# Kernel optimization log

Hardware: AMD Instinct MI355X
Metric: run time of the kernel (lower is better)

Reference implementation:

```python
import jax, jax.numpy as jnp
import numpy as np

B, S, D, H = 2, 2048, 1024, 16
HD = D // H  # head_dim = 64
INIT_STD = 0.02


def rotate_half(x):
    half = x.shape[-1] // 2
    return jnp.concatenate((-x[..., half:], x[..., :half]), axis=-1)


def setup_inputs() -> dict:
    key = jax.random.key(0)
    ks = jax.random.split(key, 6)
    inputs_q = jax.random.normal(ks[0], (B, S, D), dtype=jnp.float32)
    # causal mask, shape [B, 1, S, S] (broadcasts over heads)
    mask = jnp.broadcast_to(jnp.tril(jnp.ones((S, S), dtype=bool))[None, None], (B, 1, S, S))
    Wq = jax.random.normal(ks[1], (D, D), dtype=jnp.float32) * INIT_STD
    Wk = jax.random.normal(ks[2], (D, D), dtype=jnp.float32) * INIT_STD
    Wv = jax.random.normal(ks[3], (D, D), dtype=jnp.float32) * INIT_STD
    Wo = jax.random.normal(ks[4], (D, D), dtype=jnp.float32) * INIT_STD
    bq = jnp.zeros((D,), jnp.float32)
    bk = jnp.zeros((D,), jnp.float32)
    bv = jnp.zeros((D,), jnp.float32)
    bo = jnp.zeros((D,), jnp.float32)
    return {"inputs_q": inputs_q, "mask": mask, "Wq": Wq, "bq": bq, "Wk": Wk, "bk": bk,
            "Wv": Wv, "bv": bv, "Wo": Wo, "bo": bo}


def reference(inputs_q, mask, Wq, bq, Wk, bk, Wv, bv, Wo, bo):
    b, s, d = inputs_q.shape
    h, hd = H, d // H
    # QKV projections, split heads -> [b, s, h, hd]
    q = (inputs_q @ Wq + bq).reshape(b, s, h, hd)
    k = (inputs_q @ Wk + bk).reshape(b, s, h, hd)
    v = (inputs_q @ Wv + bv).reshape(b, s, h, hd)
    # rotary position embedding (GPT-J/Llama style: duplicated freqs over halves)
    pos = jnp.arange(s, dtype=jnp.float32)
    inv_freq = 1.0 / (10000.0 ** (jnp.arange(0, hd, 2, dtype=jnp.float32) / hd))
    freqs = pos[:, None] * inv_freq[None, :]              # [s, hd//2]
    emb = jnp.concatenate((freqs, freqs), axis=-1)        # [s, hd]
    sin = jnp.sin(emb)[None, :, None, :]                  # [1, s, 1, hd]
    cos = jnp.cos(emb)[None, :, None, :]
    q = q * cos + rotate_half(q) * sin
    k = k * cos + rotate_half(k) * sin
    # additive attention bias from boolean mask
    bias = jnp.where(mask, 0.0, jnp.finfo(jnp.float32).min)  # [b, 1, s, s]
    scores = jnp.einsum('bqhd,bkhd->bhqk', q, k) / jnp.sqrt(jnp.float32(hd)) + bias
    attn = jax.nn.softmax(scores, axis=-1)                   # [b, h, q, k]
    out = jnp.einsum('bhqk,bkhd->bqhd', attn, v).reshape(b, s, d)
    return out @ Wo + bo
```

## Files before the change

kernel.cpp:

```cpp
#include <hip/hip_runtime.h>
#include <math.h>

typedef unsigned short u16;
typedef unsigned int   u32;
typedef __attribute__((ext_vector_type(8))) short bf16x8;
typedef __attribute__((ext_vector_type(4))) short s16x4;
typedef __attribute__((ext_vector_type(4))) float f32x4;

#define BB 2
#define SS 2048
#define DD 1024
#define HH 16
#define HD 64
#define MM (BB*SS)
#define QKVN 3072

__device__ __forceinline__ u16 f2bf(float f) {
    u32 u = __float_as_uint(f);
    return (u16)((u + 0x7fffu + ((u >> 16) & 1u)) >> 16);
}
__device__ __forceinline__ float bf2f(u16 h) {
    return __uint_as_float(((u32)h) << 16);
}
__device__ __forceinline__ u32 cvt_pk_bf16(float lo, float hi) {
    u32 r;
    asm("v_cvt_pk_bf16_f32 %0, %1, %2" : "=v"(r) : "v"(lo), "v"(hi));
    return r;
}
__device__ __forceinline__ void gload16(const void* g, void* l) {
    __builtin_amdgcn_global_load_lds(
        (const __attribute__((address_space(1))) u32*)g,
        (__attribute__((address_space(3))) u32*)l, 16, 0, 0);
}

__global__ __launch_bounds__(256) void prep_kernel(
        const float* __restrict__ x,
        const float* __restrict__ W0, const float* __restrict__ W1,
        const float* __restrict__ W2, const float* __restrict__ W3,
        const float* __restrict__ b0, const float* __restrict__ b1,
        const float* __restrict__ b2,
        u16* __restrict__ Xb,
        u16* __restrict__ T0, u16* __restrict__ T1,
        u16* __restrict__ T2, u16* __restrict__ T3,
        float* __restrict__ bcat) {
    const int t = threadIdx.x;

    if (blockIdx.z == 4) {
        const int bid = blockIdx.y * 16 + blockIdx.x;
        #pragma unroll 4
        for (int it = 0; it < 16; ++it) {
            int i = (bid * 16 + it) * 256 + t;
            float4 v = reinterpret_cast<const float4*>(x)[i];
            u32 lo = (u32)f2bf(v.x) | ((u32)f2bf(v.y) << 16);
            u32 hi = (u32)f2bf(v.z) | ((u32)f2bf(v.w) << 16);
            reinterpret_cast<uint2*>(Xb)[i] = make_uint2(lo, hi);
        }
        if (bid < 12) {
            int i = bid * 256 + t;
            bcat[i] = (i < 1024) ? b0[i] : (i < 2048) ? b1[i - 1024] : b2[i - 2048];
        }
        return;
    }

    const float* W; u16* T;
    switch (blockIdx.z) {
        case 0:  W = W0; T = T0; break;
        case 1:  W = W1; T = T1; break;
        case 2:  W = W2; T = T2; break;
        default: W = W3; T = T3; break;
    }
    __shared__ float L[64][65];
    const int k0 = blockIdx.x * 64, n0 = blockIdx.y * 64;
    #pragma unroll
    for (int rep = 0; rep < 4; ++rep) {
        int row = rep * 16 + (t >> 4);
        int col = (t & 15) * 4;
        float4 v = *reinterpret_cast<const float4*>(&W[(size_t)(k0 + row) * DD + n0 + col]);
        L[row][col] = v.x; L[row][col+1] = v.y; L[row][col+2] = v.z; L[row][col+3] = v.w;
    }
    __syncthreads();
    #pragma unroll
    for (int rep = 0; rep < 2; ++rep) {
        int q  = t + rep * 256;
        int n  = q >> 3, sl = q & 7;
        u32 w[4];
        #pragma unroll
        for (int e = 0; e < 4; ++e) {
            float a = L[sl*8 + 2*e][n];
            float b = L[sl*8 + 2*e + 1][n];
            w[e] = (u32)f2bf(a) | ((u32)f2bf(b) << 16);
        }
        *reinterpret_cast<uint4*>(&T[(size_t)(n0 + n) * DD + k0 + sl*8]) =
            make_uint4(w[0], w[1], w[2], w[3]);
    }
}

template <typename OT, int BN, bool ROPE>
__global__ __launch_bounds__(256, 3) void gemm_bf16(
        const u16* __restrict__ A, const u16* __restrict__ Bt,
        const float* __restrict__ bias, OT* __restrict__ C, int N) {
    constexpr int K = DD;
    constexpr int NJ = BN / 32;
    __shared__ __align__(16) u16 As[2][128 * 32];
    __shared__ __align__(16) u16 Bs[2][BN * 32];
    const int tid  = threadIdx.x;
    const int lane = tid & 63, w = tid >> 6;
    const int g = lane >> 4, c = lane & 15;
    const int wr = w >> 1, wc = w & 1;
    const int rowbase = blockIdx.x * 128;
    const int colbase = blockIdx.y * BN;

    auto stage = [&](int t, int bf) {
        const int k0 = t * 32;
        #pragma unroll
        for (int i = 0; i < 2; ++i) {
            int row = w * 32 + i * 16 + (lane >> 2);
            int sl  = lane & 3;
            gload16(&A [(size_t)(rowbase + row) * K + k0 + sl * 8],
                    &As[bf][(w * 32 + i * 16) * 32]);
        }
        #pragma unroll
        for (int i = 0; i < BN / 64; ++i) {
            int rb  = w * (BN / 4) + i * 16;
            int row = rb + (lane >> 2);
            int sl  = lane & 3;
            gload16(&Bt[(size_t)(colbase + row) * K + k0 + sl * 8],
                    &Bs[bf][rb * 32]);
        }
    };

    f32x4 acc[4][NJ];
    #pragma unroll
    for (int i = 0; i < 4; ++i)
        #pragma unroll
        for (int j = 0; j < NJ; ++j) acc[i][j] = (f32x4){0.f, 0.f, 0.f, 0.f};

    stage(0, 0);
    __syncthreads();

    for (int t = 0; t < K / 32; ++t) {
        const int cur = t & 1;
        if (t + 1 < K / 32) stage(t + 1, cur ^ 1);
        bf16x8 af[4], bfr[NJ];
        #pragma unroll
        for (int mi = 0; mi < 4; ++mi)
            af[mi] = *reinterpret_cast<const bf16x8*>(
                &As[cur][(wr * 64 + mi * 16 + c) * 32 + g * 8]);
        #pragma unroll
        for (int nj = 0; nj < NJ; ++nj)
            bfr[nj] = *reinterpret_cast<const bf16x8*>(
                &Bs[cur][(wc * (BN / 2) + nj * 16 + c) * 32 + g * 8]);
        #pragma unroll
        for (int mi = 0; mi < 4; ++mi)
            #pragma unroll
            for (int nj = 0; nj < NJ; ++nj)
                acc[mi][nj] = __builtin_amdgcn_mfma_f32_16x16x32_bf16(
                    af[mi], bfr[nj], acc[mi][nj], 0, 0, 0);
        __syncthreads();
    }

    if constexpr (ROPE) {
        const int region = colbase >> 10;
        const float invf0 = exp2f(-0.41524101186f * (float)c);
        const float invf1 = exp2f(-0.41524101186f * (float)(16 + c));
        #pragma unroll
        for (int mi = 0; mi < 4; ++mi)
            #pragma unroll
            for (int r = 0; r < 4; ++r) {
                const int rowg = rowbase + wr * 64 + mi * 16 + g * 4 + r;
                const float s = (float)(rowg & (SS - 1));
                #pragma unroll
                for (int nj = 0; nj < 2; ++nj) {
                    const int col_lo = colbase + wc * 64 + nj * 16 + c;
                    float lo = acc[mi][nj][r]     + bias[col_lo];
                    float hi = acc[mi][nj + 2][r] + bias[col_lo + 32];
                    if (region < 2) {
                        const float f = s * (nj ? invf1 : invf0);
                        float sn, cs;
                        __sincosf(f, &sn, &cs);
                        float rlo = lo * cs - hi * sn;
                        float rhi = hi * cs + lo * sn;
                        if (region == 0) { rlo *= 0.125f; rhi *= 0.125f; }
                        lo = rlo; hi = rhi;
                    }
                    C[(size_t)rowg * N + col_lo]      = (OT)f2bf(lo);
                    C[(size_t)rowg * N + col_lo + 32] = (OT)f2bf(hi);
                }
            }
    } else {
        #pragma unroll
        for (int mi = 0; mi < 4; ++mi)
            #pragma unroll
            for (int nj = 0; nj < NJ; ++nj) {
                int colg = colbase + wc * (BN / 2) + nj * 16 + c;
                float bv = bias[colg];
                #pragma unroll
                for (int r = 0; r < 4; ++r) {
                    int rowg = rowbase + wr * 64 + mi * 16 + g * 4 + r;
                    float v = acc[mi][nj][r] + bv;
                    if constexpr (sizeof(OT) == 2) C[(size_t)rowg * N + colg] = (OT)f2bf(v);
                    else                           C[(size_t)rowg * N + colg] = v;
                }
            }
    }
}

__global__ __launch_bounds__(512) void attn_mfma(
        const u16* __restrict__ qb, const u16* __restrict__ kb,
        const u16* __restrict__ vb, u16* __restrict__ ob) {
    const int bid = blockIdx.x;
    const int bh  = bid & 31;
    const int p   = bid >> 5;
    const int b   = bh >> 4, h = bh & 15;
    const int tid = threadIdx.x;
    const int lane = tid & 63, wq = tid >> 6;
    const int g = lane >> 4, c = lane & 15;
    const int qg = wq & 3;
    const int kg = wq >> 2;

    __shared__ u16 Ks[2][2][64 * 64];
    __shared__ u16 Vt[2][2][64 * 66];
    __shared__ float Mrg[4][64][36];

    const int krow = tid >> 3;
    const int ksl  = tid & 7;

    auto load_tile = [&](int kt, uint4& kr, uint4& vr) {
        const size_t base = (size_t)(b * SS + kt * 64 + krow) * QKVN + h * 64 + ksl * 8;
        kr = *reinterpret_cast<const uint4*>(&kb[base]);
        vr = *reinterpret_cast<const uint4*>(&vb[base]);
    };
    auto write_tile = [&](int pb, int s, const uint4& kr, const uint4& vr) {
        *reinterpret_cast<uint4*>(&Ks[pb][s][krow * 64 + ((ksl ^ (krow & 7)) * 8)]) = kr;
        u32 ww[4] = {vr.x, vr.y, vr.z, vr.w};
        #pragma unroll
        for (int e = 0; e < 4; ++e) {
            Vt[pb][s][(ksl * 8 + 2 * e    ) * 66 + krow] = (u16)(ww[e] & 0xffffu);
            Vt[pb][s][(ksl * 8 + 2 * e + 1) * 66 + krow] = (u16)(ww[e] >> 16);
        }
    };

    for (int half = 0; half < 2; ++half) {
        const int qt  = half ? p : (15 - p);
        const int qw0 = qt * 128 + qg * 32;
        const int nkt = qt * 2 + 2;

        bf16x8 qf[2][2];
        #pragma unroll
        for (int nj = 0; nj < 2; ++nj)
            #pragma unroll
            for (int ks = 0; ks < 2; ++ks)
                qf[nj][ks] = *reinterpret_cast<const bf16x8*>(
                    &qb[(size_t)(b * SS + qw0 + nj*16 + c) * QKVN + h*64 + ks*32 + g*8]);

        f32x4 of[4][2];
        #pragma unroll
        for (int i = 0; i < 4; ++i)
            #pragma unroll
            for (int j = 0; j < 2; ++j) of[i][j] = (f32x4){0.f, 0.f, 0.f, 0.f};
        float mv[2] = {-1e30f, -1e30f};
        float lv[2] = {0.f, 0.f};

        auto compute_tile = [&](int kt, int pbuf, int slot) {
            const int k0 = kt * 64;
            f32x4 sf[4][2];
            #pragma unroll
            for (int i = 0; i < 4; ++i)
                #pragma unroll
                for (int j = 0; j < 2; ++j) sf[i][j] = (f32x4){0.f, 0.f, 0.f, 0.f};
            __builtin_amdgcn_s_setprio(1);
            #pragma unroll
            for (int ks = 0; ks < 2; ++ks)
                #pragma unroll
                for (int mi = 0; mi < 4; ++mi) {
                    int row = mi*16 + c;
                    bf16x8 kf = *reinterpret_cast<const bf16x8*>(
                        &Ks[pbuf][slot][row*64 + (((ks*4 + g) ^ (row & 7)) * 8)]);
                    #pragma unroll
                    for (int nj = 0; nj < 2; ++nj)
                        sf[mi][nj] = __builtin_amdgcn_mfma_f32_16x16x32_bf16(
                            kf, qf[nj][ks], sf[mi][nj], 0, 0, 0);
                }
            __builtin_amdgcn_s_setprio(0);

            if (k0 + 64 > qw0) {
                #pragma unroll
                for (int mi = 0; mi < 4; ++mi) {
                    int key = k0 + mi*16 + g*4;
                    #pragma unroll
                    for (int nj = 0; nj < 2; ++nj) {
                        int qv = qw0 + nj*16 + c;
                        #pragma unroll
                        for (int r = 0; r < 4; ++r)
                            if (key + r > qv) sf[mi][nj][r] = -1e30f;
                    }
                }
            }

            union PB { u32 u[4]; bf16x8 v; } pb2[2][2];
            #pragma unroll
            for (int nj = 0; nj < 2; ++nj) {
                float pmax = -1e30f;
                #pragma unroll
                for (int mi = 0; mi < 4; ++mi)
                    #pragma unroll
                    for (int r = 0; r < 4; ++r) pmax = fmaxf(pmax, sf[mi][nj][r]);
                pmax = fmaxf(pmax, __shfl_xor(pmax, 16));
                pmax = fmaxf(pmax, __shfl_xor(pmax, 32));
                if (!__all(pmax - mv[nj] <= 8.0f)) {
                    float mnew = fmaxf(mv[nj], pmax);
                    float corr = __expf(mv[nj] - mnew);
                    mv[nj] = mnew;
                    lv[nj] *= corr;
                    #pragma unroll
                    for (int mid = 0; mid < 4; ++mid) of[mid][nj] *= corr;
                }
                float pp[4][4]; float ls = 0.f;
                #pragma unroll
                for (int mi = 0; mi < 4; ++mi)
                    #pragma unroll
                    for (int r = 0; r < 4; ++r) {
                        float e = __expf(sf[mi][nj][r] - mv[nj]);
                        pp[mi][r] = e; ls += e;
                    }
                ls += __shfl_xor(ls, 16);
                ls += __shfl_xor(ls, 32);
                lv[nj] += ls;
                #pragma unroll
                for (int ks = 0; ks < 2; ++ks) {
                    pb2[nj][ks].u[0] = cvt_pk_bf16(pp[2*ks][0],     pp[2*ks][1]);
                    pb2[nj][ks].u[1] = cvt_pk_bf16(pp[2*ks][2],     pp[2*ks][3]);
                    pb2[nj][ks].u[2] = cvt_pk_bf16(pp[2*ks + 1][0], pp[2*ks + 1][1]);
                    pb2[nj][ks].u[3] = cvt_pk_bf16(pp[2*ks + 1][2], pp[2*ks + 1][3]);
                }
            }

            __builtin_amdgcn_s_setprio(1);
            #pragma unroll
            for (int mid = 0; mid < 4; ++mid) {
                int d = mid*16 + c;
                #pragma unroll
                for (int ks = 0; ks < 2; ++ks) {
                    union { s16x4 hh[2]; bf16x8 v; } vv;
                    vv.hh[0] = *reinterpret_cast<const s16x4*>(&Vt[pbuf][slot][d*66 + ks*32 + 4*g]);
                    vv.hh[1] = *reinterpret_cast<const s16x4*>(&Vt[pbuf][slot][d*66 + ks*32 + 16 + 4*g]);
                    #pragma unroll
                    for (int nj = 0; nj < 2; ++nj)
                        of[mid][nj] = __builtin_amdgcn_mfma_f32_16x16x32_bf16(
                            vv.v, pb2[nj][ks].v, of[mid][nj], 0, 0, 0);
                }
            }
            __builtin_amdgcn_s_setprio(0);
        };

        uint4 k0A, v0A, k1A, v1A, k0B, v0B, k1B, v1B;

        auto phase = [&](int ph,
                         uint4& kW0, uint4& vW0, uint4& kW1, uint4& vW1,
                         uint4& kL0, uint4& vL0, uint4& kL1, uint4& vL1) {
            const int cur = ph & 1;
            const int t0 = ph * 2;
            if (t0 + 4 < nkt) {
                load_tile(t0 + 4, kL0, vL0);
                load_tile(t0 + 5, kL1, vL1);
            }
            __syncthreads();
            const int myt = t0 + kg;
            if (myt * 64 <= qw0 + 31) compute_tile(myt, cur, kg);
            if (t0 + 2 < nkt) {
                write_tile(cur ^ 1, 0, kW0, vW0);
                write_tile(cur ^ 1, 1, kW1, vW1);
            }
        };

        load_tile(0, k0A, v0A);
        load_tile(1, k1A, v1A);
        __syncthreads();
        write_tile(0, 0, k0A, v0A);
        write_tile(0, 1, k1A, v1A);
        if (2 < nkt) { load_tile(2, k0B, v0B); load_tile(3, k1B, v1B); }

        const int nph = nkt >> 1;
        for (int ph = 0; ph + 1 < nph; ph += 2) {
            phase(ph,     k0B, v0B, k1B, v1B, k0A, v0A, k1A, v1A);
            phase(ph + 1, k0A, v0A, k1A, v1A, k0B, v0B, k1B, v1B);
        }
        if (nph & 1)
            phase(nph - 1, k0B, v0B, k1B, v1B, k0A, v0A, k1A, v1A);

        __syncthreads();
        if (kg == 1) {
            float* m = &Mrg[qg][lane][0];
            m[0] = mv[0]; m[1] = mv[1]; m[2] = lv[0]; m[3] = lv[1];
            #pragma unroll
            for (int mid = 0; mid < 4; ++mid)
                #pragma unroll
                for (int nj = 0; nj < 2; ++nj)
                    #pragma unroll
                    for (int r = 0; r < 4; ++r)
                        m[4 + mid*8 + nj*4 + r] = of[mid][nj][r];
        }
        __syncthreads();
        if (kg == 0) {
            const float* m1 = &Mrg[qg][lane][0];
            #pragma unroll
            for (int nj = 0; nj < 2; ++nj) {
                float mB = m1[nj];
                float mm = fmaxf(mv[nj], mB);
                float c0 = __expf(mv[nj] - mm);
                float c1 = __expf(mB - mm);
                float ll = lv[nj] * c0 + m1[2 + nj] * c1;
                float inv = 1.0f / ll;
                int qv = qw0 + nj*16 + c;
                #pragma unroll
                for (int mid = 0; mid < 4; ++mid) {
                    float o0 = (of[mid][nj][0]*c0 + m1[4 + mid*8 + nj*4 + 0]*c1) * inv;
                    float o1 = (of[mid][nj][1]*c0 + m1[4 + mid*8 + nj*4 + 1]*c1) * inv;
                    float o2 = (of[mid][nj][2]*c0 + m1[4 + mid*8 + nj*4 + 2]*c1) * inv;
                    float o3 = (of[mid][nj][3]*c0 + m1[4 + mid*8 + nj*4 + 3]*c1) * inv;
                    *reinterpret_cast<uint2*>(
                        &ob[(size_t)(b * SS + qv) * DD + h*64 + mid*16 + g*4]) =
                        make_uint2(cvt_pk_bf16(o0, o1), cvt_pk_bf16(o2, o3));
                }
            }
        }
    }
}

extern "C" void kernel_launch(void* const* d_in, const int* in_sizes, int n_in,
                              void* d_out, int out_size, void* d_ws, size_t ws_size,
                              hipStream_t stream) {
    const float* x  = (const float*)d_in[0];
    const float* Wq = (const float*)d_in[2];
    const float* bq = (const float*)d_in[3];
    const float* Wk = (const float*)d_in[4];
    const float* bk = (const float*)d_in[5];
    const float* Wv = (const float*)d_in[6];
    const float* bv = (const float*)d_in[7];
    const float* Wo = (const float*)d_in[8];
    const float* bo = (const float*)d_in[9];
    float* out = (float*)d_out;

    u16* Xb   = (u16*)d_ws;
    u16* Wcat = Xb   + (size_t)MM * DD;
    u16* Wot  = Wcat + (size_t)3 * DD * DD;
    u16* qkv  = Wot  + (size_t)DD * DD;
    u16* abuf = qkv  + (size_t)MM * QKVN;
    float* bcat = (float*)(abuf + (size_t)MM * DD);

    prep_kernel<<<dim3(16, 16, 5), 256, 0, stream>>>(
        x, Wq, Wk, Wv, Wo, bq, bk, bv,
        Xb, Wcat, Wcat + (size_t)DD * DD, Wcat + (size_t)2 * DD * DD, Wot, bcat);

    gemm_bf16<u16, 128, true><<<dim3(32, 24), 256, 0, stream>>>(Xb, Wcat, bcat, qkv, QKVN);

    attn_mfma<<<256, 512, 0, stream>>>(qkv, qkv + 1024, qkv + 2048, abuf);

    gemm_bf16<float, 64, false><<<dim3(32, 16), 256, 0, stream>>>(abuf, Wot, bo, out, DD);
}
```

Measured before the change: 108.2 us.

## Split attention into one query tile per block and alias LDS buffers

Each attention block now processes a single query tile instead of a paired long/short tile, doubling the grid to 512 blocks ordered from longest to shortest causal work. K/V staging buffers and the merge scratch are placed in one shared pool, with the merge area aliased onto K/V storage to cut LDS use. Launch bounds now request higher occupancy. This aims for better load balance and latency hiding, but relies on the hardware scheduler for balance and duplicates the per-block Q loads and setup.

```diff
diff --git a/kernel.cpp b/kernel.cpp
--- a/kernel.cpp
+++ b/kernel.cpp
@@ -205,12 +205,12 @@
     }
 }
 
-__global__ __launch_bounds__(512) void attn_mfma(
+__global__ __launch_bounds__(512, 4) void attn_mfma(
         const u16* __restrict__ qb, const u16* __restrict__ kb,
         const u16* __restrict__ vb, u16* __restrict__ ob) {
     const int bid = blockIdx.x;
     const int bh  = bid & 31;
-    const int p   = bid >> 5;
+    const int qt  = 15 - (bid >> 5);
     const int b   = bh >> 4, h = bh & 15;
     const int tid = threadIdx.x;
     const int lane = tid & 63, wq = tid >> 6;
@@ -218,9 +218,10 @@
     const int qg = wq & 3;
     const int kg = wq >> 2;
 
-    __shared__ u16 Ks[2][2][64 * 64];
-    __shared__ u16 Vt[2][2][64 * 66];
-    __shared__ float Mrg[4][64][36];
+    __shared__ __align__(16) u16 pool[4 * 64 * 64 + 4 * 64 * 66];
+    auto KsP = [&](int pb, int s) -> u16* { return pool + (pb * 2 + s) * (64 * 64); };
+    auto VtP = [&](int pb, int s) -> u16* { return pool + 4 * 64 * 64 + (pb * 2 + s) * (64 * 66); };
+    float* MrgBase = reinterpret_cast<float*>(pool);
 
     const int krow = tid >> 3;
     const int ksl  = tid & 7;
@@ -231,197 +232,196 @@
         vr = *reinterpret_cast<const uint4*>(&vb[base]);
     };
     auto write_tile = [&](int pb, int s, const uint4& kr, const uint4& vr) {
-        *reinterpret_cast<uint4*>(&Ks[pb][s][krow * 64 + ((ksl ^ (krow & 7)) * 8)]) = kr;
+        *reinterpret_cast<uint4*>(&KsP(pb, s)[krow * 64 + ((ksl ^ (krow & 7)) * 8)]) = kr;
+        u16* vt = VtP(pb, s);
         u32 ww[4] = {vr.x, vr.y, vr.z, vr.w};
         #pragma unroll
         for (int e = 0; e < 4; ++e) {
-            Vt[pb][s][(ksl * 8 + 2 * e    ) * 66 + krow] = (u16)(ww[e] & 0xffffu);
-            Vt[pb][s][(ksl * 8 + 2 * e + 1) * 66 + krow] = (u16)(ww[e] >> 16);
+            vt[(ksl * 8 + 2 * e    ) * 66 + krow] = (u16)(ww[e] & 0xffffu);
+            vt[(ksl * 8 + 2 * e + 1) * 66 + krow] = (u16)(ww[e] >> 16);
         }
     };
 
-    for (int half = 0; half < 2; ++half) {
-        const int qt  = half ? p : (15 - p);
-        const int qw0 = qt * 128 + qg * 32;
-        const int nkt = qt * 2 + 2;
-
-        bf16x8 qf[2][2];
-        #pragma unroll
-        for (int nj = 0; nj < 2; ++nj)
-            #pragma unroll
-            for (int ks = 0; ks < 2; ++ks)
-                qf[nj][ks] = *reinterpret_cast<const bf16x8*>(
-                    &qb[(size_t)(b * SS + qw0 + nj*16 + c) * QKVN + h*64 + ks*32 + g*8]);
-
-        f32x4 of[4][2];
+    const int qw0 = qt * 128 + qg * 32;
+    const int nkt = qt * 2 + 2;
+
+    bf16x8 qf[2][2];
+    #pragma unroll
+    for (int nj = 0; nj < 2; ++nj)
+        #pragma unroll
+        for (int ks = 0; ks < 2; ++ks)
+            qf[nj][ks] = *reinterpret_cast<const bf16x8*>(
+                &qb[(size_t)(b * SS + qw0 + nj*16 + c) * QKVN + h*64 + ks*32 + g*8]);
+
+    f32x4 of[4][2];
+    #pragma unroll
+    for (int i = 0; i < 4; ++i)
+        #pragma unroll
+        for (int j = 0; j < 2; ++j) of[i][j] = (f32x4){0.f, 0.f, 0.f, 0.f};
+    float mv[2] = {-1e30f, -1e30f};
+    float lv[2] = {0.f, 0.f};
+
+    auto compute_tile = [&](int kt, int pbuf, int slot) {
+        const int k0 = kt * 64;
+        const u16* ks_t = KsP(pbuf, slot);
+        const u16* vt_t = VtP(pbuf, slot);
+        f32x4 sf[4][2];
         #pragma unroll
         for (int i = 0; i < 4; ++i)
             #pragma unroll
-            for (int j = 0; j < 2; ++j) of[i][j] = (f32x4){0.f, 0.f, 0.f, 0.f};
-        float mv[2] = {-1e30f, -1e30f};
-        float lv[2] = {0.f, 0.f};
-
-        auto compute_tile = [&](int kt, int pbuf, int slot) {
-            const int k0 = kt * 64;
-            f32x4 sf[4][2];
-            #pragma unroll
-            for (int i = 0; i < 4; ++i)
-                #pragma unroll
-                for (int j = 0; j < 2; ++j) sf[i][j] = (f32x4){0.f, 0.f, 0.f, 0.f};
-            __builtin_amdgcn_s_setprio(1);
-            #pragma unroll
-            for (int ks = 0; ks < 2; ++ks)
-                #pragma unroll
-                for (int mi = 0; mi < 4; ++mi) {
-                    int row = mi*16 + c;
-                    bf16x8 kf = *reinterpret_cast<const bf16x8*>(
-                        &Ks[pbuf][slot][row*64 + (((ks*4 + g) ^ (row & 7)) * 8)]);
-                    #pragma unroll
-                    for (int nj = 0; nj < 2; ++nj)
-                        sf[mi][nj] = __builtin_amdgcn_mfma_f32_16x16x32_bf16(
-                            kf, qf[nj][ks], sf[mi][nj], 0, 0, 0);
-                }
-            __builtin_amdgcn_s_setprio(0);
-
-            if (k0 + 64 > qw0) {
-                #pragma unroll
-                for (int mi = 0; mi < 4; ++mi) {
-                    int key = k0 + mi*16 + g*4;
-                    #pragma unroll
-                    for (int nj = 0; nj < 2; ++nj) {
-                        int qv = qw0 + nj*16 + c;
-                        #pragma unroll
-                        for (int r = 0; r < 4; ++r)
-                            if (key + r > qv) sf[mi][nj][r] = -1e30f;
-                    }
-                }
-            }
-
-            union PB { u32 u[4]; bf16x8 v; } pb2[2][2];
-            #pragma unroll
-            for (int nj = 0; nj < 2; ++nj) {
-                float pmax = -1e30f;
-                #pragma unroll
-                for (int mi = 0; mi < 4; ++mi)
-                    #pragma unroll
-                    for (int r = 0; r < 4; ++r) pmax = fmaxf(pmax, sf[mi][nj][r]);
-                pmax = fmaxf(pmax, __shfl_xor(pmax, 16));
-                pmax = fmaxf(pmax, __shfl_xor(pmax, 32));
-                if (!__all(pmax - mv[nj] <= 8.0f)) {
-                    float mnew = fmaxf(mv[nj], pmax);
-                    float corr = __expf(mv[nj] - mnew);
-                    mv[nj] = mnew;
-                    lv[nj] *= corr;
-                    #pragma unroll
-                    for (int mid = 0; mid < 4; ++mid) of[mid][nj] *= corr;
-                }
-                float pp[4][4]; float ls = 0.f;
-                #pragma unroll
-                for (int mi = 0; mi < 4; ++mi)
-                    #pragma unroll
-                    for (int r = 0; r < 4; ++r) {
-                        float e = __expf(sf[mi][nj][r] - mv[nj]);
-                        pp[mi][r] = e; ls += e;
-                    }
-                ls += __shfl_xor(ls, 16);
-                ls += __shfl_xor(ls, 32);
-                lv[nj] += ls;
-                #pragma unroll
-                for (int ks = 0; ks < 2; ++ks) {
-                    pb2[nj][ks].u[0] = cvt_pk_bf16(pp[2*ks][0],     pp[2*ks][1]);
-                    pb2[nj][ks].u[1] = cvt_pk_bf16(pp[2*ks][2],     pp[2*ks][3]);
-                    pb2[nj][ks].u[2] = cvt_pk_bf16(pp[2*ks + 1][0], pp[2*ks + 1][1]);
-                    pb2[nj][ks].u[3] = cvt_pk_bf16(pp[2*ks + 1][2], pp[2*ks + 1][3]);
-                }
-            }
-
-            __builtin_amdgcn_s_setprio(1);
-            #pragma unroll
-            for (int mid = 0; mid < 4; ++mid) {
-                int d = mid*16 + c;
-                #pragma unroll
-                for (int ks = 0; ks < 2; ++ks) {
-                    union { s16x4 hh[2]; bf16x8 v; } vv;
-                    vv.hh[0] = *reinterpret_cast<const s16x4*>(&Vt[pbuf][slot][d*66 + ks*32 + 4*g]);
-                    vv.hh[1] = *reinterpret_cast<const s16x4*>(&Vt[pbuf][slot][d*66 + ks*32 + 16 + 4*g]);
-                    #pragma unroll
-                    for (int nj = 0; nj < 2; ++nj)
-                        of[mid][nj] = __builtin_amdgcn_mfma_f32_16x16x32_bf16(
-                            vv.v, pb2[nj][ks].v, of[mid][nj], 0, 0, 0);
-                }
-            }
-            __builtin_amdgcn_s_setprio(0);
-        };
-
-        uint4 k0A, v0A, k1A, v1A, k0B, v0B, k1B, v1B;
-
-        auto phase = [&](int ph,
-                         uint4& kW0, uint4& vW0, uint4& kW1, uint4& vW1,
-                         uint4& kL0, uint4& vL0, uint4& kL1, uint4& vL1) {
-            const int cur = ph & 1;
-            const int t0 = ph * 2;
-            if (t0 + 4 < nkt) {
-                load_tile(t0 + 4, kL0, vL0);
-                load_tile(t0 + 5, kL1, vL1);
-            }
-            __syncthreads();
-            const int myt = t0 + kg;
-            if (myt * 64 <= qw0 + 31) compute_tile(myt, cur, kg);
-            if (t0 + 2 < nkt) {
-                write_tile(cur ^ 1, 0, kW0, vW0);
-                write_tile(cur ^ 1, 1, kW1, vW1);
-            }
-        };
-
-        load_tile(0, k0A, v0A);
-        load_tile(1, k1A, v1A);
-        __syncthreads();
-        write_tile(0, 0, k0A, v0A);
-        write_tile(0, 1, k1A, v1A);
-        if (2 < nkt) { load_tile(2, k0B, v0B); load_tile(3, k1B, v1B); }
-
-        const int nph = nkt >> 1;
-        for (int ph = 0; ph + 1 < nph; ph += 2) {
-            phase(ph,     k0B, v0B, k1B, v1B, k0A, v0A, k1A, v1A);
-            phase(ph + 1, k0A, v0A, k1A, v1A, k0B, v0B, k1B, v1B);
-        }
-        if (nph & 1)
-            phase(nph - 1, k0B, v0B, k1B, v1B, k0A, v0A, k1A, v1A);
-
-        __syncthreads();
-        if (kg == 1) {
-            float* m = &Mrg[qg][lane][0];
-            m[0] = mv[0]; m[1] = mv[1]; m[2] = lv[0]; m[3] = lv[1];
-            #pragma unroll
-            for (int mid = 0; mid < 4; ++mid)
+            for (int j = 0; j < 2; ++j) sf[i][j] = (f32x4){0.f, 0.f, 0.f, 0.f};
+        __builtin_amdgcn_s_setprio(1);
+        #pragma unroll
+        for (int ks = 0; ks < 2; ++ks)
+            #pragma unroll
+            for (int mi = 0; mi < 4; ++mi) {
+                int row = mi*16 + c;
+                bf16x8 kf = *reinterpret_cast<const bf16x8*>(
+                    &ks_t[row*64 + (((ks*4 + g) ^ (row & 7)) * 8)]);
                 #pragma unroll
                 for (int nj = 0; nj < 2; ++nj)
+                    sf[mi][nj] = __builtin_amdgcn_mfma_f32_16x16x32_bf16(
+                        kf, qf[nj][ks], sf[mi][nj], 0, 0, 0);
+            }
+        __builtin_amdgcn_s_setprio(0);
+
+        if (k0 + 64 > qw0) {
+            #pragma unroll
+            for (int mi = 0; mi < 4; ++mi) {
+                int key = k0 + mi*16 + g*4;
+                #pragma unroll
+                for (int nj = 0; nj < 2; ++nj) {
+                    int qv = qw0 + nj*16 + c;
                     #pragma unroll
                     for (int r = 0; r < 4; ++r)
-                        m[4 + mid*8 + nj*4 + r] = of[mid][nj][r];
+                        if (key + r > qv) sf[mi][nj][r] = -1e30f;
+                }
+            }
+        }
+
+        union PB { u32 u[4]; bf16x8 v; } pb2[2][2];
+        #pragma unroll
+        for (int nj = 0; nj < 2; ++nj) {
+            float pmax = -1e30f;
+            #pragma unroll
+            for (int mi = 0; mi < 4; ++mi)
+                #pragma unroll
+                for (int r = 0; r < 4; ++r) pmax = fmaxf(pmax, sf[mi][nj][r]);
+            pmax = fmaxf(pmax, __shfl_xor(pmax, 16));
+            pmax = fmaxf(pmax, __shfl_xor(pmax, 32));
+            if (!__all(pmax - mv[nj] <= 8.0f)) {
+                float mnew = fmaxf(mv[nj], pmax);
+                float corr = __expf(mv[nj] - mnew);
+                mv[nj] = mnew;
+                lv[nj] *= corr;
+                #pragma unroll
+                for (int mid = 0; mid < 4; ++mid) of[mid][nj] *= corr;
+            }
+            float pp[4][4]; float ls = 0.f;
+            #pragma unroll
+            for (int mi = 0; mi < 4; ++mi)
+                #pragma unroll
+                for (int r = 0; r < 4; ++r) {
+                    float e = __expf(sf[mi][nj][r] - mv[nj]);
+                    pp[mi][r] = e; ls += e;
+                }
+            ls += __shfl_xor(ls, 16);
+            ls += __shfl_xor(ls, 32);
+            lv[nj] += ls;
+            #pragma unroll
+            for (int ks = 0; ks < 2; ++ks) {
+                pb2[nj][ks].u[0] = cvt_pk_bf16(pp[2*ks][0],     pp[2*ks][1]);
+                pb2[nj][ks].u[1] = cvt_pk_bf16(pp[2*ks][2],     pp[2*ks][3]);
+                pb2[nj][ks].u[2] = cvt_pk_bf16(pp[2*ks + 1][0], pp[2*ks + 1][1]);
+                pb2[nj][ks].u[3] = cvt_pk_bf16(pp[2*ks + 1][2], pp[2*ks + 1][3]);
+            }
+        }
+
+        __builtin_amdgcn_s_setprio(1);
+        #pragma unroll
+        for (int mid = 0; mid < 4; ++mid) {
+            int d = mid*16 + c;
+            #pragma unroll
+            for (int ks = 0; ks < 2; ++ks) {
+                union { s16x4 hh[2]; bf16x8 v; } vv;
+                vv.hh[0] = *reinterpret_cast<const s16x4*>(&vt_t[d*66 + ks*32 + 4*g]);
+                vv.hh[1] = *reinterpret_cast<const s16x4*>(&vt_t[d*66 + ks*32 + 16 + 4*g]);
+                #pragma unroll
+                for (int nj = 0; nj < 2; ++nj)
+                    of[mid][nj] = __builtin_amdgcn_mfma_f32_16x16x32_bf16(
+                        vv.v, pb2[nj][ks].v, of[mid][nj], 0, 0, 0);
+            }
+        }
+        __builtin_amdgcn_s_setprio(0);
+    };
+
+    uint4 k0A, v0A, k1A, v1A, k0B, v0B, k1B, v1B;
+
+    auto phase = [&](int ph,
+                     uint4& kW0, uint4& vW0, uint4& kW1, uint4& vW1,
+                     uint4& kL0, uint4& vL0, uint4& kL1, uint4& vL1) {
+        const int cur = ph & 1;
+        const int t0 = ph * 2;
+        if (t0 + 4 < nkt) {
+            load_tile(t0 + 4, kL0, vL0);
+            load_tile(t0 + 5, kL1, vL1);
         }
         __syncthreads();
-        if (kg == 0) {
-            const float* m1 = &Mrg[qg][lane][0];
-            #pragma unroll
-            for (int nj = 0; nj < 2; ++nj) {
-                float mB = m1[nj];
-                float mm = fmaxf(mv[nj], mB);
-                float c0 = __expf(mv[nj] - mm);
-                float c1 = __expf(mB - mm);
-                float ll = lv[nj] * c0 + m1[2 + nj] * c1;
-                float inv = 1.0f / ll;
-                int qv = qw0 + nj*16 + c;
-                #pragma unroll
-                for (int mid = 0; mid < 4; ++mid) {
-                    float o0 = (of[mid][nj][0]*c0 + m1[4 + mid*8 + nj*4 + 0]*c1) * inv;
-                    float o1 = (of[mid][nj][1]*c0 + m1[4 + mid*8 + nj*4 + 1]*c1) * inv;
-                    float o2 = (of[mid][nj][2]*c0 + m1[4 + mid*8 + nj*4 + 2]*c1) * inv;
-                    float o3 = (of[mid][nj][3]*c0 + m1[4 + mid*8 + nj*4 + 3]*c1) * inv;
-                    *reinterpret_cast<uint2*>(
-                        &ob[(size_t)(b * SS + qv) * DD + h*64 + mid*16 + g*4]) =
-                        make_uint2(cvt_pk_bf16(o0, o1), cvt_pk_bf16(o2, o3));
-                }
+        const int myt = t0 + kg;
+        if (myt * 64 <= qw0 + 31) compute_tile(myt, cur, kg);
+        if (t0 + 2 < nkt) {
+            write_tile(cur ^ 1, 0, kW0, vW0);
+            write_tile(cur ^ 1, 1, kW1, vW1);
+        }
+    };
+
+    load_tile(0, k0A, v0A);
+    load_tile(1, k1A, v1A);
+    write_tile(0, 0, k0A, v0A);
+    write_tile(0, 1, k1A, v1A);
+    if (2 < nkt) { load_tile(2, k0B, v0B); load_tile(3, k1B, v1B); }
+
+    const int nph = nkt >> 1;
+    for (int ph = 0; ph + 1 < nph; ph += 2) {
+        phase(ph,     k0B, v0B, k1B, v1B, k0A, v0A, k1A, v1A);
+        phase(ph + 1, k0A, v0A, k1A, v1A, k0B, v0B, k1B, v1B);
+    }
+    if (nph & 1)
+        phase(nph - 1, k0B, v0B, k1B, v1B, k0A, v0A, k1A, v1A);
+
+    __syncthreads();
+    if (kg == 1) {
+        float* m = &MrgBase[(qg * 64 + lane) * 36];
+        m[0] = mv[0]; m[1] = mv[1]; m[2] = lv[0]; m[3] = lv[1];
+        #pragma unroll
+        for (int mid = 0; mid < 4; ++mid)
+            #pragma unroll
+            for (int nj = 0; nj < 2; ++nj)
+                #pragma unroll
+                for (int r = 0; r < 4; ++r)
+                    m[4 + mid*8 + nj*4 + r] = of[mid][nj][r];
+    }
+    __syncthreads();
+    if (kg == 0) {
+        const float* m1 = &MrgBase[(qg * 64 + lane) * 36];
+        #pragma unroll
+        for (int nj = 0; nj < 2; ++nj) {
+            float mB = m1[nj];
+            float mm = fmaxf(mv[nj], mB);
+            float c0 = __expf(mv[nj] - mm);
+            float c1 = __expf(mB - mm);
+            float ll = lv[nj] * c0 + m1[2 + nj] * c1;
+            float inv = 1.0f / ll;
+            int qv = qw0 + nj*16 + c;
+            #pragma unroll
+            for (int mid = 0; mid < 4; ++mid) {
+                float o0 = (of[mid][nj][0]*c0 + m1[4 + mid*8 + nj*4 + 0]*c1) * inv;
+                float o1 = (of[mid][nj][1]*c0 + m1[4 + mid*8 + nj*4 + 1]*c1) * inv;
+                float o2 = (of[mid][nj][2]*c0 + m1[4 + mid*8 + nj*4 + 2]*c1) * inv;
+                float o3 = (of[mid][nj][3]*c0 + m1[4 + mid*8 + nj*4 + 3]*c1) * inv;
+                *reinterpret_cast<uint2*>(
+                    &ob[(size_t)(b * SS + qv) * DD + h*64 + mid*16 + g*4]) =
+                    make_uint2(cvt_pk_bf16(o0, o1), cvt_pk_bf16(o2, o3));
             }
         }
     }
@@ -454,7 +454,7 @@
 
     gemm_bf16<u16, 128, true><<<dim3(32, 24), 256, 0, stream>>>(Xb, Wcat, bcat, qkv, QKVN);
 
-    attn_mfma<<<256, 512, 0, stream>>>(qkv, qkv + 1024, qkv + 2048, abuf);
+    attn_mfma<<<512, 512, 0, stream>>>(qkv, qkv + 1024, qkv + 2048, abuf);
 
     gemm_bf16<float, 64, false><<<dim3(32, 16), 256, 0, stream>>>(abuf, Wot, bo, out, DD);
 }
```

New measurement: 194.1 us. +79.4%, slower.
